# Performance work log

Hardware: AMD Instinct MI355X
Metric: run time of the kernel (lower is better)

## Reference

```python
import jax, jax.numpy as jnp
import numpy as np

B, C, H, W = 8, 64, 256, 256
DW = 2 * C          # dw_channel
FFN = 2 * C         # ffn_channel
EPS = 1e-6


def setup_inputs() -> dict:
    key = jax.random.key(0)
    ks = jax.random.split(key, 16)
    f = lambda k, s, scale=1.0: (jax.random.normal(k, s, jnp.float32) * scale)
    return {
        "inp": f(ks[0], (B, C, H, W)),
        "w1": f(ks[1], (B, DW, C, 1, 1)),
        "b1": f(ks[2], (B, DW), 0.01),
        "w2": f(ks[3], (B, DW, 1, 3, 3)),
        "b2": f(ks[4], (B, DW), 0.01),
        "w3": f(ks[5], (B, C, DW // 2, 1, 1)),
        "b3": f(ks[6], (B, C), 0.01),
        "w4": f(ks[7], (B, FFN, C, 1, 1)),
        "b4": f(ks[8], (B, FFN), 0.01),
        "w5": f(ks[9], (B, C, FFN // 2, 1, 1)),
        "b5": f(ks[10], (B, C), 0.01),
        "ln1_w": jnp.ones((C,), jnp.float32),
        "ln1_b": jnp.zeros((C,), jnp.float32),
        "ln2_w": jnp.ones((C,), jnp.float32),
        "ln2_b": jnp.zeros((C,), jnp.float32),
        "sca_w": f(ks[11], (DW // 2, DW // 2, 1, 1), 0.05),
        "sca_b": jnp.zeros((DW // 2,), jnp.float32),
        "beta": f(ks[12], (1, C, 1, 1), 0.1),
        "gamma": f(ks[13], (1, C, 1, 1), 0.1),
    }


def _layernorm2d(x, w, b):
    # LayerNorm over channel dim per pixel (NAFNet LayerNorm2d)
    mu = jnp.mean(x, axis=1, keepdims=True)
    var = jnp.var(x, axis=1, keepdims=True)
    xn = (x - mu) * jax.lax.rsqrt(var + EPS)
    return xn * w[None, :, None, None] + b[None, :, None, None]


def _normalize_weights(w):
    # w: [B, co, ci, kh, kw]; Frobenius norm over (ci, kh, kw) per (b, co)
    nrm = jnp.sqrt(jnp.sum(w * w, axis=(2, 3, 4), keepdims=True))
    return w / nrm


def _pw(x, w, b):
    # per-sample 1x1 conv: x [B,ci,H,W], w [B,co,ci,1,1], b [B,co]
    return jnp.einsum("bchw,boc->bohw", x, w[:, :, :, 0, 0]) + b[:, :, None, None]


def _dw3x3(x, w, b):
    # per-sample depthwise 3x3: x [B,DW,H,W], w [B,DW,1,3,3], b [B,DW]
    def one(xi, wi):
        y = jax.lax.conv_general_dilated(
            xi[None], wi, window_strides=(1, 1), padding="SAME",
            dimension_numbers=("NCHW", "OIHW", "NCHW"),
            feature_group_count=DW)
        return y[0]
    return jax.vmap(one)(x, w) + b[:, :, None, None]


def _simple_gate(x):
    x1, x2 = jnp.split(x, 2, axis=1)
    return x1 * x2


def reference(inp, w1, b1, w2, b2, w3, b3, w4, b4, w5, b5,
              ln1_w, ln1_b, ln2_w, ln2_b, sca_w, sca_b, beta, gamma):
    x = _layernorm2d(inp, ln1_w, ln1_b)
    x = _pw(x, _normalize_weights(w1), b1)          # [B,DW,H,W]
    x = _dw3x3(x, _normalize_weights(w2), b2)       # [B,DW,H,W]
    x = _simple_gate(x)                             # [B,DW/2,H,W]
    pooled = jnp.mean(x, axis=(2, 3))               # [B,DW/2]
    sca = jnp.einsum("bc,oc->bo", pooled, sca_w[:, :, 0, 0]) + sca_b
    x = x * sca[:, :, None, None]
    x = _pw(x, _normalize_weights(w3), b3)          # [B,C,H,W]
    y = inp + x * beta
    x = _layernorm2d(y, ln2_w, ln2_b)
    x = _pw(x, _normalize_weights(w4), b4)          # [B,FFN,H,W]
    x = _simple_gate(x)                             # [B,FFN/2,H,W]
    x = _pw(x, _normalize_weights(w5), b5)          # [B,C,H,W]
    return y + x * gamma
```

## Files before the change

kernel.cpp:

```cpp
#include <hip/hip_runtime.h>
#include <hip/hip_bf16.h>

typedef __attribute__((ext_vector_type(8))) short short8;
typedef __attribute__((ext_vector_type(4))) float f32x4;

#define HWN 65536
#define WN 256
#define HN 256

#define HALO_W 34
#define HALO_N 340
#define MT_N 22

#define W2N_OFF 0
#define W1BF_OFF 9216
#define W3BF_OFF 41984
#define W4BF_OFF 58368
#define W5BF_OFF 91136
#define POOL_OFF 107520
#define SCA_OFF 108032

static __device__ __forceinline__ short f2bs(float f) {
    union { __hip_bfloat16 h; short s; } u; u.h = __float2bfloat16(f); return u.s;
}
static __device__ __forceinline__ float bs2f(short s) {
    union { unsigned u; float f; } v; v.u = ((unsigned)(unsigned short)s) << 16; return v.f;
}

__device__ __forceinline__ void norm_row(const float* __restrict__ in,
                                         float* __restrict__ out, int n) {
    float s = 0.f;
    for (int i = 0; i < n; i++) { float v = in[i]; s += v * v; }
    float r = rsqrtf(s);
    for (int i = 0; i < n; i++) out[i] = in[i] * r;
}

__device__ __forceinline__ void norm_row_bf(const float* __restrict__ in,
                                            short* __restrict__ out, int n) {
    float s = 0.f;
    for (int i = 0; i < n; i++) { float v = in[i]; s += v * v; }
    float r = rsqrtf(s);
    for (int i = 0; i < n; i++) out[i] = f2bs(in[i] * r);
}

__global__ void k_prep(const float* __restrict__ w1, const float* __restrict__ w2,
                       const float* __restrict__ w3, const float* __restrict__ w4,
                       const float* __restrict__ w5, float* __restrict__ ws) {
    int r = blockIdx.x * 256 + threadIdx.x;
    short* w1bf = (short*)(ws + W1BF_OFF);
    short* w3bf = (short*)(ws + W3BF_OFF);
    short* w4bf = (short*)(ws + W4BF_OFF);
    short* w5bf = (short*)(ws + W5BF_OFF);
    if (r < 1024) {
        norm_row_bf(w1 + r * 64, w1bf + r * 64, 64);
    } else if (r < 2048) {
        int rr = r - 1024;
        norm_row(w2 + rr * 9, ws + W2N_OFF + rr * 9, 9);
    } else if (r < 2560) {
        int rr = r - 2048;
        norm_row_bf(w3 + rr * 64, w3bf + rr * 64, 64);
    } else if (r < 3584) {
        int rr = r - 2560;
        norm_row_bf(w4 + rr * 64, w4bf + rr * 64, 64);
    } else if (r < 4096) {
        int rr = r - 3584;
        norm_row_bf(w5 + rr * 64, w5bf + rr * 64, 64);
    } else if (r < 4608) {
        ws[POOL_OFF + (r - 4096)] = 0.f;
    }
}

__global__ __launch_bounds__(256, 3) void k1(
    const float* __restrict__ inp, const float* __restrict__ ln1w,
    const float* __restrict__ ln1b, const float* __restrict__ b1,
    const float* __restrict__ b2v, const float* __restrict__ ws,
    float* __restrict__ g, float* __restrict__ pooled) {
    const short* w1bf = (const short*)(ws + W1BF_OFF);
    const float* w2n = ws + W2N_OFF;
    const int b = blockIdx.x >> 8;
    const int tile = blockIdx.x & 255;
    const int x0 = (tile & 7) << 5, y0 = (tile >> 3) << 3;
    const int t = threadIdx.x;
    const int wave = t >> 6, lane = t & 63;
    const int n = lane & 15, q = lane >> 4;

    __shared__ float sPA[2][HALO_N * 8];
    __shared__ float sPB[2][HALO_N * 8];
    __shared__ float sRed[8 * 4 * 8];

    float wc[16], bc[16];
#pragma unroll
    for (int j = 0; j < 8; j++) {
        wc[j] = ln1w[q * 8 + j];
        bc[j] = ln1b[q * 8 + j];
        wc[8 + j] = ln1w[32 + q * 8 + j];
        bc[8 + j] = ln1b[32 + q * 8 + j];
    }

    short8 afr0[6], afr1[6];
    const float* xbase = inp + ((size_t)b << 22);
    float va[16], vb[16];

#define LOADX(dst, I)                                                         \
    if (wave + (I) * 4 < MT_N) {                                              \
        int pix = (wave + (I) * 4) * 16 + n;                                  \
        int hy = pix / HALO_W, hx = pix - hy * HALO_W;                        \
        int yy = y0 - 1 + hy, xx = x0 - 1 + hx;                               \
        bool inb = ((unsigned)yy < HN) && ((unsigned)xx < WN) &&              \
                   (pix < HALO_N);                                            \
        const float* xin = xbase + (yy * WN + xx);                            \
        _Pragma("unroll")                                                     \
        for (int j = 0; j < 8; j++) {                                         \
            dst[j]     = inb ? xin[(size_t)(q * 8 + j) << 16] : 0.f;          \
            dst[8 + j] = inb ? xin[(size_t)(32 + q * 8 + j) << 16] : 0.f;     \
        }                                                                     \
    }

#define LNX(src, I)                                                           \
    if (wave + (I) * 4 < MT_N) {                                              \
        float s = 0.f, s2 = 0.f;                                              \
        _Pragma("unroll")                                                     \
        for (int j = 0; j < 16; j++) { s += src[j]; s2 += src[j] * src[j]; }  \
        s += __shfl_xor(s, 16); s += __shfl_xor(s, 32);                       \
        s2 += __shfl_xor(s2, 16); s2 += __shfl_xor(s2, 32);                   \
        float mu = s * (1.f / 64.f);                                          \
        float var = s2 * (1.f / 64.f) - mu * mu;                              \
        float rr = rsqrtf(var + 1e-6f);                                       \
        short8 a0, a1;                                                        \
        _Pragma("unroll")                                                     \
        for (int j = 0; j < 8; j++) {                                         \
            a0[j] = f2bs((src[j] - mu) * rr * wc[j] + bc[j]);                 \
            a1[j] = f2bs((src[8 + j] - mu) * rr * wc[8 + j] + bc[8 + j]);     \
        }                                                                     \
        afr0[(I)] = a0; afr1[(I)] = a1;                                       \
    }

    LOADX(va, 0)
    LOADX(vb, 1)
    LNX(va, 0)
    LOADX(va, 2)
    LNX(vb, 1)
    LOADX(vb, 3)
    LNX(va, 2)
    LOADX(va, 4)
    LNX(vb, 3)
    LOADX(vb, 5)
    LNX(va, 4)
    LNX(vb, 5)
#undef LOADX
#undef LNX

    unsigned vmask = 0;
#pragma unroll
    for (int i = 0; i < 6; i++) {
        int mt = wave + i * 4;
        if (mt < MT_N) {
#pragma unroll
            for (int r = 0; r < 4; r++) {
                int row = mt * 16 + q * 4 + r;
                int hy = row / HALO_W, hx = row - hy * HALO_W;
                int yy = y0 - 1 + hy, xx = x0 - 1 + hx;
                if (row < HALO_N && ((unsigned)yy < HN) && ((unsigned)xx < WN))
                    vmask |= 1u << (i * 4 + r);
            }
        }
    }

    const short* w1b = w1bf + b * 128 * 64;
    const float* w2b = w2n + b * 128 * 9;
    const float* b1b = b1 + b * 128;
    const float* b2b = b2v + b * 128;
    const int lx = t & 31, ly = t >> 5;

    for (int cc = 0; cc < 8; cc++) {
        int outch = cc * 8 + (n < 8 ? n : 56 + n);
        short8 bf0 = *(const short8*)(w1b + outch * 64 + q * 8);
        short8 bf1 = *(const short8*)(w1b + outch * 64 + 32 + q * 8);
        float bias = b1b[outch];
        float* spA = sPA[cc & 1];
        float* spB = sPB[cc & 1];
#pragma unroll
        for (int i = 0; i < 6; i++) {
            int mt = wave + i * 4;
            if (mt < MT_N) {
                f32x4 d = {0.f, 0.f, 0.f, 0.f};
                d = __builtin_amdgcn_mfma_f32_16x16x32_bf16(afr0[i], bf0, d, 0, 0, 0);
                d = __builtin_amdgcn_mfma_f32_16x16x32_bf16(afr1[i], bf1, d, 0, 0, 0);
#pragma unroll
                for (int r = 0; r < 4; r++) {
                    int row = mt * 16 + q * 4 + r;
                    float val = ((vmask >> (i * 4 + r)) & 1u) ? (d[r] + bias) : 0.f;
                    if (row < HALO_N) {
                        if (n < 8) spA[row * 8 + n] = val;
                        else       spB[row * 8 + (n - 8)] = val;
                    }
                }
            }
        }
        __syncthreads();
        float accA[8], accB[8];
#pragma unroll
        for (int p = 0; p < 8; p++) {
            accA[p] = b2b[cc * 8 + p];
            accB[p] = b2b[64 + cc * 8 + p];
        }
#pragma unroll
        for (int ky = 0; ky < 3; ky++) {
#pragma unroll
            for (int kx = 0; kx < 3; kx++) {
                int e = (ly + ky) * HALO_W + lx + kx;
                f32x4 a0v = *(const f32x4*)&spA[e * 8];
                f32x4 a1v = *(const f32x4*)&spA[e * 8 + 4];
                f32x4 b0v = *(const f32x4*)&spB[e * 8];
                f32x4 b1v = *(const f32x4*)&spB[e * 8 + 4];
                const float* wA = w2b + (cc * 8) * 9 + ky * 3 + kx;
                const float* wB = w2b + (64 + cc * 8) * 9 + ky * 3 + kx;
#pragma unroll
                for (int p = 0; p < 4; p++) {
                    accA[p]     += a0v[p] * wA[p * 9];
                    accA[p + 4] += a1v[p] * wA[(p + 4) * 9];
                    accB[p]     += b0v[p] * wB[p * 9];
                    accB[p + 4] += b1v[p] * wB[(p + 4) * 9];
                }
            }
        }
        float v[8];
        size_t gbase = ((size_t)(b * 64 + cc * 8)) * HWN + (size_t)((y0 + ly) * WN + x0 + lx);
#pragma unroll
        for (int p = 0; p < 8; p++) {
            v[p] = accA[p] * accB[p];
            g[gbase + ((size_t)p << 16)] = v[p];
        }
#pragma unroll
        for (int p = 0; p < 8; p++) {
            float s = v[p];
            s += __shfl_xor(s, 1);  s += __shfl_xor(s, 2);
            s += __shfl_xor(s, 4);  s += __shfl_xor(s, 8);
            s += __shfl_xor(s, 16); s += __shfl_xor(s, 32);
            if (lane == 0) sRed[(cc * 4 + wave) * 8 + p] = s;
        }
    }
    __syncthreads();
    if (t < 64) {
        int cc = t >> 3, p = t & 7;
        float s = sRed[(cc * 4 + 0) * 8 + p] + sRed[(cc * 4 + 1) * 8 + p] +
                  sRed[(cc * 4 + 2) * 8 + p] + sRed[(cc * 4 + 3) * 8 + p];
        atomicAdd(&pooled[b * 64 + cc * 8 + p], s);
    }
}

__global__ void k_sca(const float* __restrict__ pooled,
                      const float* __restrict__ scaw,
                      const float* __restrict__ scab,
                      float* __restrict__ sca) {
    int t = threadIdx.x;
    int b = t >> 6, o = t & 63;
    float acc = scab[o];
    for (int c = 0; c < 64; c++)
        acc += pooled[b * 64 + c] * (1.f / 65536.f) * scaw[o * 64 + c];
    sca[t] = acc;
}

__global__ __launch_bounds__(256, 4) void k2(
    const float* __restrict__ inp, const float* g, const float* __restrict__ ws,
    const float* __restrict__ b3, const float* __restrict__ beta,
    const float* __restrict__ ln2w, const float* __restrict__ ln2b,
    const float* __restrict__ b4, const float* __restrict__ b5,
    const float* __restrict__ gamma, float* out) {
    const int b = blockIdx.x >> 9;
    const int px0 = (blockIdx.x & 511) << 7;
    const int t = threadIdx.x;
    const int wave = t >> 6, lane = t & 63;
    const int n = lane & 15, q = lane >> 4;

    __shared__ short sX[128 * 72];
    __shared__ short sB[128 * 72];

    const float* scav = ws + SCA_OFF + b * 64;

    {
        const float* gb = g + ((size_t)b << 22) + px0;
        for (int i2 = t; i2 < 2048; i2 += 256) {
            int c = i2 >> 5, pxg = i2 & 31;
            f32x4 v = *(const f32x4*)&gb[((size_t)c << 16) + pxg * 4];
            float sc = scav[c];
#pragma unroll
            for (int r = 0; r < 4; r++)
                sX[(pxg * 4 + r) * 72 + c] = f2bs(v[r] * sc);
        }
    }
    __syncthreads();

    float yreg[4][2][4];
    {
        const short* w3b = (const short*)(ws + W3BF_OFF) + b * 64 * 64;
        const float* b3b = b3 + b * 64;
        short8 a0h[2], a1h[2];
#pragma unroll
        for (int mi = 0; mi < 2; mi++) {
            const short* arow = &sX[((wave + mi * 4) * 16 + n) * 72];
            a0h[mi] = *(const short8*)(arow + q * 8);
            a1h[mi] = *(const short8*)(arow + 32 + q * 8);
        }
#pragma unroll
        for (int nc = 0; nc < 4; nc++) {
            int outch = nc * 16 + n;
            short8 bf0 = *(const short8*)(w3b + outch * 64 + q * 8);
            short8 bf1 = *(const short8*)(w3b + outch * 64 + 32 + q * 8);
            float b3v = b3b[outch], betav = beta[outch];
            const float* ib = inp + ((size_t)b << 22) + ((size_t)outch << 16) + px0;
#pragma unroll
            for (int mi = 0; mi < 2; mi++) {
                int mt = wave + mi * 4;
                f32x4 d = {0.f, 0.f, 0.f, 0.f};
                d = __builtin_amdgcn_mfma_f32_16x16x32_bf16(a0h[mi], bf0, d, 0, 0, 0);
                d = __builtin_amdgcn_mfma_f32_16x16x32_bf16(a1h[mi], bf1, d, 0, 0, 0);
                f32x4 resid = *(const f32x4*)(ib + mt * 16 + q * 4);
#pragma unroll
                for (int r = 0; r < 4; r++) {
                    float y = resid[r] + betav * (d[r] + b3v);
                    yreg[nc][mi][r] = y;
                    sB[(mt * 16 + q * 4 + r) * 72 + outch] = f2bs(y);
                }
            }
        }
    }
    __syncthreads();

    {
        int px = t >> 1, half = t & 1;
        const short* yrow = &sB[px * 72 + half * 32];
        short8 yv[4];
        float s = 0.f, s2 = 0.f;
#pragma unroll
        for (int v8 = 0; v8 < 4; v8++) {
            yv[v8] = *(const short8*)(yrow + v8 * 8);
#pragma unroll
            for (int j = 0; j < 8; j++) {
                float f = bs2f(yv[v8][j]);
                s += f; s2 += f * f;
            }
        }
        s += __shfl_xor(s, 1); s2 += __shfl_xor(s2, 1);
        float mu = s * (1.f / 64.f);
        float var = s2 * (1.f / 64.f) - mu * mu;
        float rr = rsqrtf(var + 1e-6f);
        short* xrow = &sX[px * 72 + half * 32];
#pragma unroll
        for (int v8 = 0; v8 < 4; v8++) {
            short8 o;
#pragma unroll
            for (int j = 0; j < 8; j++) {
                int c = half * 32 + v8 * 8 + j;
                o[j] = f2bs((bs2f(yv[v8][j]) - mu) * rr * ln2w[c] + ln2b[c]);
            }
            *(short8*)(xrow + v8 * 8) = o;
        }
    }
    __syncthreads();

    {
        const short* w4b = (const short*)(ws + W4BF_OFF) + b * 128 * 64;
        const float* b4b = b4 + b * 128;
        short8 a0h[2], a1h[2];
#pragma unroll
        for (int mi = 0; mi < 2; mi++) {
            const short* arow = &sX[((wave + mi * 4) * 16 + n) * 72];
            a0h[mi] = *(const short8*)(arow + q * 8);
            a1h[mi] = *(const short8*)(arow + 32 + q * 8);
        }
        for (int cc = 0; cc < 8; cc++) {
            int outch = cc * 8 + (n < 8 ? n : 56 + n);
            short8 bf0 = *(const short8*)(w4b + outch * 64 + q * 8);
            short8 bf1 = *(const short8*)(w4b + outch * 64 + 32 + q * 8);
            float b4v = b4b[outch];
#pragma unroll
            for (int mi = 0; mi < 2; mi++) {
                int mt = wave + mi * 4;
                f32x4 d = {0.f, 0.f, 0.f, 0.f};
                d = __builtin_amdgcn_mfma_f32_16x16x32_bf16(a0h[mi], bf0, d, 0, 0, 0);
                d = __builtin_amdgcn_mfma_f32_16x16x32_bf16(a1h[mi], bf1, d, 0, 0, 0);
#pragma unroll
                for (int r = 0; r < 4; r++) {
                    float val = d[r] + b4v;
                    float other = __shfl_xor(val, 8);
                    if (n < 8)
                        sB[(mt * 16 + q * 4 + r) * 72 + cc * 8 + n] = f2bs(val * other);
                }
            }
        }
    }
    __syncthreads();

    {
        const short* w5b = (const short*)(ws + W5BF_OFF) + b * 64 * 64;
        const float* b5b = b5 + b * 64;
        float* ob = out + ((size_t)b << 22) + px0;
        short8 a0h[2], a1h[2];
#pragma unroll
        for (int mi = 0; mi < 2; mi++) {
            const short* arow = &sB[((wave + mi * 4) * 16 + n) * 72];
            a0h[mi] = *(const short8*)(arow + q * 8);
            a1h[mi] = *(const short8*)(arow + 32 + q * 8);
        }
#pragma unroll
        for (int nc = 0; nc < 4; nc++) {
            int outch = nc * 16 + n;
            short8 bf0 = *(const short8*)(w5b + outch * 64 + q * 8);
            short8 bf1 = *(const short8*)(w5b + outch * 64 + 32 + q * 8);
            float b5v = b5b[outch], gam = gamma[outch];
#pragma unroll
            for (int mi = 0; mi < 2; mi++) {
                int mt = wave + mi * 4;
                f32x4 d = {0.f, 0.f, 0.f, 0.f};
                d = __builtin_amdgcn_mfma_f32_16x16x32_bf16(a0h[mi], bf0, d, 0, 0, 0);
                d = __builtin_amdgcn_mfma_f32_16x16x32_bf16(a1h[mi], bf1, d, 0, 0, 0);
                f32x4 o;
#pragma unroll
                for (int r = 0; r < 4; r++)
                    o[r] = yreg[nc][mi][r] + gam * (d[r] + b5v);
                *(f32x4*)(ob + ((size_t)outch << 16) + mt * 16 + q * 4) = o;
            }
        }
    }
}

extern "C" void kernel_launch(void* const* d_in, const int* in_sizes, int n_in,
                              void* d_out, int out_size, void* d_ws, size_t ws_size,
                              hipStream_t stream) {
    const float* inp  = (const float*)d_in[0];
    const float* w1   = (const float*)d_in[1];
    const float* b1   = (const float*)d_in[2];
    const float* w2   = (const float*)d_in[3];
    const float* b2v  = (const float*)d_in[4];
    const float* w3   = (const float*)d_in[5];
    const float* b3   = (const float*)d_in[6];
    const float* w4   = (const float*)d_in[7];
    const float* b4   = (const float*)d_in[8];
    const float* w5   = (const float*)d_in[9];
    const float* b5   = (const float*)d_in[10];
    const float* ln1w = (const float*)d_in[11];
    const float* ln1b = (const float*)d_in[12];
    const float* ln2w = (const float*)d_in[13];
    const float* ln2b = (const float*)d_in[14];
    const float* scaw = (const float*)d_in[15];
    const float* scab = (const float*)d_in[16];
    const float* beta = (const float*)d_in[17];
    const float* gamma= (const float*)d_in[18];

    float* ws = (float*)d_ws;
    float* pooled = ws + POOL_OFF;
    float* sca = ws + SCA_OFF;
    float* g = (float*)d_out;
    float* out = (float*)d_out;

    k_prep<<<17, 256, 0, stream>>>(w1, w2, w3, w4, w5, ws);
    k1<<<2048, 256, 0, stream>>>(inp, ln1w, ln1b, b1, b2v, ws, g, pooled);
    k_sca<<<1, 512, 0, stream>>>(pooled, scaw, scab, sca);
    k2<<<4096, 256, 0, stream>>>(inp, g, ws, b3, beta, ln2w, ln2b, b4, b5,
                                 gamma, out);
}
```

Measured before the change: 608.8 us.

## Store k1 pointwise halo in bf16 LDS and fold SCA computation into k2

The intermediate 1x1-conv output tile in k1 shared memory changes from fp32 to bf16. This halves LDS footprint and read traffic for the depthwise 3x3, which may allow higher occupancy. Separately, the k_sca launch is removed: each k2 block recomputes the 64-element channel attention vector from pooled sums into shared memory. That drops one kernel launch at the cost of redundant per-block work and an extra barrier. The bf16 rounding adds a small precision loss before the depthwise conv.

```diff
diff --git a/kernel.cpp b/kernel.cpp
--- a/kernel.cpp
+++ b/kernel.cpp
@@ -18,7 +18,6 @@
 #define W4BF_OFF 58368
 #define W5BF_OFF 91136
 #define POOL_OFF 107520
-#define SCA_OFF 108032
 
 static __device__ __forceinline__ short f2bs(float f) {
     union { __hip_bfloat16 h; short s; } u; u.h = __float2bfloat16(f); return u.s;
@@ -84,8 +83,8 @@
     const int wave = t >> 6, lane = t & 63;
     const int n = lane & 15, q = lane >> 4;
 
-    __shared__ float sPA[2][HALO_N * 8];
-    __shared__ float sPB[2][HALO_N * 8];
+    __shared__ short sPA[2][HALO_N * 8];
+    __shared__ short sPB[2][HALO_N * 8];
     __shared__ float sRed[8 * 4 * 8];
 
     float wc[16], bc[16];
@@ -177,8 +176,8 @@
         short8 bf0 = *(const short8*)(w1b + outch * 64 + q * 8);
         short8 bf1 = *(const short8*)(w1b + outch * 64 + 32 + q * 8);
         float bias = b1b[outch];
-        float* spA = sPA[cc & 1];
-        float* spB = sPB[cc & 1];
+        short* spA = sPA[cc & 1];
+        short* spB = sPB[cc & 1];
 #pragma unroll
         for (int i = 0; i < 6; i++) {
             int mt = wave + i * 4;
@@ -189,7 +188,8 @@
 #pragma unroll
                 for (int r = 0; r < 4; r++) {
                     int row = mt * 16 + q * 4 + r;
-                    float val = ((vmask >> (i * 4 + r)) & 1u) ? (d[r] + bias) : 0.f;
+                    short val = ((vmask >> (i * 4 + r)) & 1u) ? f2bs(d[r] + bias)
+                                                              : (short)0;
                     if (row < HALO_N) {
                         if (n < 8) spA[row * 8 + n] = val;
                         else       spB[row * 8 + (n - 8)] = val;
@@ -209,18 +209,12 @@
 #pragma unroll
             for (int kx = 0; kx < 3; kx++) {
                 int e = (ly + ky) * HALO_W + lx + kx;
-                f32x4 a0v = *(const f32x4*)&spA[e * 8];
-                f32x4 a1v = *(const f32x4*)&spA[e * 8 + 4];
-                f32x4 b0v = *(const f32x4*)&spB[e * 8];
-                f32x4 b1v = *(const f32x4*)&spB[e * 8 + 4];
-                const float* wA = w2b + (cc * 8) * 9 + ky * 3 + kx;
-                const float* wB = w2b + (64 + cc * 8) * 9 + ky * 3 + kx;
-#pragma unroll
-                for (int p = 0; p < 4; p++) {
-                    accA[p]     += a0v[p] * wA[p * 9];
-                    accA[p + 4] += a1v[p] * wA[(p + 4) * 9];
-                    accB[p]     += b0v[p] * wB[p * 9];
-                    accB[p + 4] += b1v[p] * wB[(p + 4) * 9];
+                short8 pA = *(const short8*)&spA[e * 8];
+                short8 pB = *(const short8*)&spB[e * 8];
+#pragma unroll
+                for (int p = 0; p < 8; p++) {
+                    accA[p] += bs2f(pA[p]) * w2b[(cc * 8 + p) * 9 + ky * 3 + kx];
+                    accB[p] += bs2f(pB[p]) * w2b[(64 + cc * 8 + p) * 9 + ky * 3 + kx];
                 }
             }
         }
@@ -249,20 +243,10 @@
     }
 }
 
-__global__ void k_sca(const float* __restrict__ pooled,
-                      const float* __restrict__ scaw,
-                      const float* __restrict__ scab,
-                      float* __restrict__ sca) {
-    int t = threadIdx.x;
-    int b = t >> 6, o = t & 63;
-    float acc = scab[o];
-    for (int c = 0; c < 64; c++)
-        acc += pooled[b * 64 + c] * (1.f / 65536.f) * scaw[o * 64 + c];
-    sca[t] = acc;
-}
-
 __global__ __launch_bounds__(256, 4) void k2(
     const float* __restrict__ inp, const float* g, const float* __restrict__ ws,
+    const float* __restrict__ pooled, const float* __restrict__ scaw,
+    const float* __restrict__ scab,
     const float* __restrict__ b3, const float* __restrict__ beta,
     const float* __restrict__ ln2w, const float* __restrict__ ln2b,
     const float* __restrict__ b4, const float* __restrict__ b5,
@@ -275,15 +259,25 @@
 
     __shared__ short sX[128 * 72];
     __shared__ short sB[128 * 72];
-
-    const float* scav = ws + SCA_OFF + b * 64;
+    __shared__ float sSca[64];
+
+    if (t < 64) {
+        float acc = scab[t];
+        const float* prow = pooled + b * 64;
+        const float* wrow = scaw + t * 64;
+#pragma unroll 8
+        for (int c = 0; c < 64; c++)
+            acc += prow[c] * (1.f / 65536.f) * wrow[c];
+        sSca[t] = acc;
+    }
+    __syncthreads();
 
     {
         const float* gb = g + ((size_t)b << 22) + px0;
         for (int i2 = t; i2 < 2048; i2 += 256) {
             int c = i2 >> 5, pxg = i2 & 31;
             f32x4 v = *(const f32x4*)&gb[((size_t)c << 16) + pxg * 4];
-            float sc = scav[c];
+            float sc = sSca[c];
 #pragma unroll
             for (int r = 0; r < 4; r++)
                 sX[(pxg * 4 + r) * 72 + c] = f2bs(v[r] * sc);
@@ -450,13 +444,11 @@
 
     float* ws = (float*)d_ws;
     float* pooled = ws + POOL_OFF;
-    float* sca = ws + SCA_OFF;
     float* g = (float*)d_out;
     float* out = (float*)d_out;
 
     k_prep<<<17, 256, 0, stream>>>(w1, w2, w3, w4, w5, ws);
     k1<<<2048, 256, 0, stream>>>(inp, ln1w, ln1b, b1, b2v, ws, g, pooled);
-    k_sca<<<1, 512, 0, stream>>>(pooled, scaw, scab, sca);
-    k2<<<4096, 256, 0, stream>>>(inp, g, ws, b3, beta, ln2w, ln2b, b4, b5,
-                                 gamma, out);
-}
+    k2<<<4096, 256, 0, stream>>>(inp, g, ws, pooled, scaw, scab, b3, beta,
+                                 ln2w, ln2b, b4, b5, gamma, out);
+}
```

Measured after the change: 586.9 us. 1.04x faster.
